# Performance work log

Hardware: AMD Instinct MI355X
Metric: run time of the kernel (lower is better)

## Reference

```python
import jax, jax.numpy as jnp
import numpy as np

B, T, S, K, H, V = 8, 100, 400, 8, 512, 32000

def setup_inputs() -> dict:
    key = jax.random.key(0)
    ks = jax.random.split(key, 8)
    return {
        "dec_out": jax.random.normal(ks[0], (B, T, H), jnp.float32),
        "W": jax.random.normal(ks[1], (H, V), jnp.float32) * (1.0 / np.sqrt(H)),
        "b": jnp.zeros((V,), jnp.float32),
        "weights": jax.random.uniform(ks[2], (B, T, S), jnp.float32),
        "p_trans": jax.random.uniform(ks[3], (B, T, 1), jnp.float32),
        "trans_probs": jax.random.uniform(ks[4], (B, S, K), jnp.float32),
        "probs": jax.random.uniform(ks[5], (B, S, K), jnp.float32),
        "idxes": jax.random.randint(ks[6], (B, S, K), 0, V, jnp.int64),
    }

def reference(dec_out, W, b, weights, p_trans, trans_probs, probs, idxes):
    # Generator: linear + softmax over vocab -> (B, T, V)
    scores = jax.nn.softmax(jnp.einsum('bth,hv->btv', dec_out, W) + b, axis=-1)
    # Mask translation probs where source prob <= 0.05
    tp = trans_probs * (probs > 0.05).astype(trans_probs.dtype)  # (B, S, K)
    # scatter_add along vocab dim: tmp[b, s, idxes[b, s, k]] += tp[b, s, k]
    bi = jnp.arange(B)[:, None, None]
    si = jnp.arange(S)[None, :, None]
    tmp = jnp.zeros((B, S, V), dec_out.dtype).at[bi, si, idxes].add(tp)
    # blend copy distribution through attention weights
    trans_scores = jnp.einsum('bts,bsv->btv', weights, tmp)
    return jnp.log(p_trans * trans_scores + (1.0 - p_trans) * scores)
```

## Files before the change

kernel.cpp:

```cpp
#include <hip/hip_runtime.h>

#define Bdim 8
#define Tdim 100
#define Sdim 400
#define Kk   8
#define Hdim 512
#define Vdim 32000
#define Mdim 800
#define VHALF 16000

typedef __attribute__((ext_vector_type(8))) short short8;
typedef __attribute__((ext_vector_type(4))) short short4v;
typedef __attribute__((ext_vector_type(4))) float float4_t;

static __device__ __forceinline__ unsigned short f2bf(float f) {
    unsigned int x = __float_as_uint(f);
    return (unsigned short)((x + 0x7fffu + ((x >> 16) & 1u)) >> 16);
}
static __device__ __forceinline__ float bf2f(unsigned short h) {
    return __uint_as_float(((unsigned int)h) << 16);
}

static __device__ __forceinline__ void gload_lds16(const void* g, void* s) {
    __builtin_amdgcn_global_load_lds((const __attribute__((address_space(1))) void*)g,
                                     (__attribute__((address_space(3))) void*)s, 16, 0, 0);
}

__global__ void zero_kernel(float* __restrict__ p, int n) {
    int i = blockIdx.x * blockDim.x + threadIdx.x;
    if (i < n) p[i] = 0.f;
}

__global__ void convert_a_kernel(const float* __restrict__ A, unsigned short* __restrict__ Abf, int n4) {
    int i = blockIdx.x * blockDim.x + threadIdx.x;
    if (i < n4) {
        float4 f = ((const float4*)A)[i];
        short4v s;
        s[0] = (short)f2bf(f.x); s[1] = (short)f2bf(f.y);
        s[2] = (short)f2bf(f.z); s[3] = (short)f2bf(f.w);
        *(short4v*)(Abf + i * 4) = s;
    }
}

__global__ __launch_bounds__(256) void transpose_kernel(const float* __restrict__ W,
                                                        unsigned short* __restrict__ WT) {
    __shared__ float tile[64][65];
    const int k0 = blockIdx.y * 64;
    const int v0 = blockIdx.x * 64;
    const int t  = threadIdx.x;
    const int tx = t & 15;
    const int ty = t >> 4;
#pragma unroll
    for (int i = 0; i < 64; i += 16) {
        float4 f = *(const float4*)&W[(size_t)(k0 + ty + i) * Vdim + v0 + tx * 4];
        tile[ty + i][tx * 4 + 0] = f.x;
        tile[ty + i][tx * 4 + 1] = f.y;
        tile[ty + i][tx * 4 + 2] = f.z;
        tile[ty + i][tx * 4 + 3] = f.w;
    }
    __syncthreads();
    const int c = t & 7;
    const int v = t >> 3;
#pragma unroll
    for (int i = 0; i < 64; i += 32) {
        short8 s;
#pragma unroll
        for (int j = 0; j < 8; ++j) s[j] = (short)f2bf(tile[c * 8 + j][v + i]);
        *(short8*)&WT[(size_t)(v0 + v + i) * Hdim + k0 + c * 8] = s;
    }
}

__global__ __launch_bounds__(256) void gemm_kernel(const unsigned short* __restrict__ Abf,
                                                   const unsigned short* __restrict__ WT,
                                                   const float* __restrict__ bias,
                                                   unsigned short* __restrict__ logitsbf,
                                                   float* __restrict__ rowsum) {
    __shared__ __align__(16) unsigned short As[2 * 128 * 64];
    __shared__ __align__(16) unsigned short Bs[2 * 128 * 64];

    const int tid  = threadIdx.x;
    const int lane = tid & 63;
    const int wave = tid >> 6;
    const int l15  = lane & 15;
    const int kq   = lane >> 4;

    const int NWG = 7 * 250;
    const int orig = blockIdx.x;
    const int xcd = orig & 7;
    const int q8  = NWG >> 3;
    const int r8  = NWG & 7;
    const int wg  = (xcd < r8 ? xcd * (q8 + 1) : r8 * (q8 + 1) + (xcd - r8) * q8) + (orig >> 3);
    const int m_blk = (wg % 7) * 128;
    const int n_blk = (wg / 7) * 128;

    const int wm = wave & 1, wn = wave >> 1;
    const int m0 = wm * 64, n0 = wn * 64;

    const unsigned short* agp[4];
    const unsigned short* bgp[4];
    int lslot[4];
#pragma unroll
    for (int q = 0; q < 4; ++q) {
        int chunk = (q * 4 + wave) * 64 + lane;
        int row = chunk >> 3, c = chunk & 7;
        int gc  = c ^ (row & 7);
        int arow = m_blk + row;
        if (arow >= Mdim) arow = Mdim - 1;
        agp[q] = Abf + (size_t)arow * Hdim + gc * 8;
        bgp[q] = WT + (size_t)(n_blk + row) * Hdim + gc * 8;
        lslot[q] = (q * 4 + wave) * 512;
    }

    int a_off[2][4], b_off[2][4];
#pragma unroll
    for (int ks = 0; ks < 2; ++ks)
#pragma unroll
        for (int i = 0; i < 4; ++i) {
            int ra = m0 + i * 16 + l15;
            a_off[ks][i] = ra * 64 + (((ks * 4 + kq) ^ (ra & 7)) * 8);
            int rb = n0 + i * 16 + l15;
            b_off[ks][i] = rb * 64 + (((ks * 4 + kq) ^ (rb & 7)) * 8);
        }

    float4_t acc[4][4] = {};

#pragma unroll
    for (int q = 0; q < 4; ++q) {
        gload_lds16(agp[q], As + lslot[q]);
        gload_lds16(bgp[q], Bs + lslot[q]);
    }
    __syncthreads();

    int cur = 0;
#pragma unroll
    for (int kt = 0; kt < 8; ++kt) {
        if (kt < 7) {
            const int ko = (kt + 1) * 64;
            const int nb = (cur ^ 1) * 8192;
#pragma unroll
            for (int q = 0; q < 4; ++q) {
                gload_lds16(agp[q] + ko, As + nb + lslot[q]);
                gload_lds16(bgp[q] + ko, Bs + nb + lslot[q]);
            }
        }
        const unsigned short* Ab = As + cur * 8192;
        const unsigned short* Bb = Bs + cur * 8192;
#pragma unroll
        for (int ks = 0; ks < 2; ++ks) {
            short8 af[4], bfr[4];
#pragma unroll
            for (int i = 0; i < 4; ++i) af[i]  = *(const short8*)(Ab + a_off[ks][i]);
#pragma unroll
            for (int j = 0; j < 4; ++j) bfr[j] = *(const short8*)(Bb + b_off[ks][j]);
#pragma unroll
            for (int i = 0; i < 4; ++i)
#pragma unroll
                for (int j = 0; j < 4; ++j)
                    acc[i][j] = __builtin_amdgcn_mfma_f32_16x16x32_bf16(af[i], bfr[j], acc[i][j], 0, 0, 0);
        }
        if (kt < 7) {
            __syncthreads();
            cur ^= 1;
        }
    }

    float bj[4];
#pragma unroll
    for (int j = 0; j < 4; ++j) bj[j] = bias[n_blk + n0 + j * 16 + l15];

#pragma unroll
    for (int i = 0; i < 4; ++i) {
        float se[4] = {0.f, 0.f, 0.f, 0.f};
        int grow0 = m_blk + m0 + i * 16 + kq * 4;
#pragma unroll
        for (int j = 0; j < 4; ++j) {
            int col = n_blk + n0 + j * 16 + l15;
#pragma unroll
            for (int r = 0; r < 4; ++r) {
                float v = acc[i][j][r] + bj[j];
                se[r] += __expf(v);
                if (grow0 + r < Mdim)
                    logitsbf[(size_t)(grow0 + r) * Vdim + col] = f2bf(v);
            }
        }
#pragma unroll
        for (int r = 0; r < 4; ++r) {
#pragma unroll
            for (int off = 8; off; off >>= 1)
                se[r] += __shfl_xor(se[r], off, 64);
        }
        if (l15 == 0) {
#pragma unroll
            for (int r = 0; r < 4; ++r)
                if (grow0 + r < Mdim) atomicAdd(&rowsum[grow0 + r], se[r]);
        }
    }
}

__global__ __launch_bounds__(512) void combine_kernel(const unsigned short* __restrict__ logitsbf,
                                                      const float* __restrict__ weights,
                                                      const float* __restrict__ p_trans,
                                                      const float* __restrict__ trans_probs,
                                                      const float* __restrict__ probs,
                                                      const int* __restrict__ idxes,
                                                      const float* __restrict__ rowsum,
                                                      float* __restrict__ out) {
    __shared__ __align__(16) float ts[VHALF];

    int bt = blockIdx.x;
    int b  = bt / Tdim;
    int tid = threadIdx.x;

    float pt = p_trans[bt];
    float c1 = (1.f - pt) / rowsum[bt];

    const short8* lrow8 = (const short8*)(logitsbf + (size_t)bt * Vdim);
    float4* out4 = (float4*)(out + (size_t)bt * Vdim);
    float4* ts4  = (float4*)ts;

    for (int h = 0; h < 2; ++h) {
        float4 z = make_float4(0.f, 0.f, 0.f, 0.f);
        for (int i = tid; i < VHALF / 4; i += 512) ts4[i] = z;
        __syncthreads();

        for (int i = tid; i < Sdim * Kk; i += 512) {
            float pv  = probs[b * (Sdim * Kk) + i];
            float tpv = trans_probs[b * (Sdim * Kk) + i];
            int   idx = idxes[b * (Sdim * Kk) + i];
            int   rel = idx - h * VHALF;
            if (pv > 0.05f && (unsigned)rel < (unsigned)VHALF) {
                float w = weights[bt * Sdim + (i >> 3)];
                atomicAdd(&ts[rel], w * tpv);
            }
        }
        __syncthreads();

        for (int i = tid; i < VHALF / 8; i += 512) {
            short8 x8 = lrow8[h * (VHALF / 8) + i];
            float4 t0 = ts4[i * 2];
            float4 t1 = ts4[i * 2 + 1];
            float4 o0, o1;
            o0.x = __logf(pt * t0.x + c1 * __expf(bf2f((unsigned short)x8[0])));
            o0.y = __logf(pt * t0.y + c1 * __expf(bf2f((unsigned short)x8[1])));
            o0.z = __logf(pt * t0.z + c1 * __expf(bf2f((unsigned short)x8[2])));
            o0.w = __logf(pt * t0.w + c1 * __expf(bf2f((unsigned short)x8[3])));
            o1.x = __logf(pt * t1.x + c1 * __expf(bf2f((unsigned short)x8[4])));
            o1.y = __logf(pt * t1.y + c1 * __expf(bf2f((unsigned short)x8[5])));
            o1.z = __logf(pt * t1.z + c1 * __expf(bf2f((unsigned short)x8[6])));
            o1.w = __logf(pt * t1.w + c1 * __expf(bf2f((unsigned short)x8[7])));
            out4[(h * (VHALF / 8) + i) * 2]     = o0;
            out4[(h * (VHALF / 8) + i) * 2 + 1] = o1;
        }
        __syncthreads();
    }
}

extern "C" void kernel_launch(void* const* d_in, const int* in_sizes, int n_in,
                              void* d_out, int out_size, void* d_ws, size_t ws_size,
                              hipStream_t stream) {
    const float* dec_out     = (const float*)d_in[0];
    const float* W           = (const float*)d_in[1];
    const float* bias        = (const float*)d_in[2];
    const float* weights     = (const float*)d_in[3];
    const float* p_trans     = (const float*)d_in[4];
    const float* trans_probs = (const float*)d_in[5];
    const float* probs       = (const float*)d_in[6];
    const int*   idxes       = (const int*)d_in[7];
    float* out = (float*)d_out;

    char* wsb = (char*)d_ws;
    unsigned short* Abf      = (unsigned short*)wsb;
    unsigned short* WT       = (unsigned short*)(wsb + (1ull << 20));
    unsigned short* logitsbf = (unsigned short*)(wsb + (35ull << 20));
    float*          rowsum   = (float*)(wsb + (90ull << 20));

    zero_kernel<<<dim3(4), dim3(256), 0, stream>>>(rowsum, Mdim);
    convert_a_kernel<<<dim3((Mdim * Hdim / 4 + 255) / 256), dim3(256), 0, stream>>>(dec_out, Abf, Mdim * Hdim / 4);
    transpose_kernel<<<dim3(Vdim / 64, Hdim / 64), dim3(256), 0, stream>>>(W, WT);
    gemm_kernel<<<dim3(7 * (Vdim / 128)), dim3(256), 0, stream>>>(Abf, WT, bias, logitsbf, rowsum);
    combine_kernel<<<dim3(Mdim), dim3(512), 0, stream>>>(logitsbf, weights, p_trans, trans_probs,
                                                         probs, idxes, rowsum, out);
}
```

Measured before the change: 284.7 us.

## Enlarge GEMM tiles to 256x256 with 512 threads and fold rowsum zeroing

The GEMM tile grows from 128x128 to 256x256, launched as 500 workgroups of 512 threads, with each wave computing a 128x64 sub-tile. The aim is to raise arithmetic intensity and cut redundant B/W reads. The per-iteration sync is rebuilt as an explicit vmcnt wait plus a barrier at the top of each k step, and A fragments are loaded one at a time to limit register pressure. The zero kernel is folded into convert_a to save a launch. The cost is more padded M rows (1024 versus 800), higher register and LDS use, and fewer workgroups to spread across CUs.

```diff
diff --git a/kernel.cpp b/kernel.cpp
--- a/kernel.cpp
+++ b/kernel.cpp
@@ -26,13 +26,10 @@
                                      (__attribute__((address_space(3))) void*)s, 16, 0, 0);
 }
 
-__global__ void zero_kernel(float* __restrict__ p, int n) {
+__global__ void convert_a_kernel(const float* __restrict__ A, unsigned short* __restrict__ Abf,
+                                 float* __restrict__ rowsum, int n4) {
     int i = blockIdx.x * blockDim.x + threadIdx.x;
-    if (i < n) p[i] = 0.f;
-}
-
-__global__ void convert_a_kernel(const float* __restrict__ A, unsigned short* __restrict__ Abf, int n4) {
-    int i = blockIdx.x * blockDim.x + threadIdx.x;
+    if (i < Mdim) rowsum[i] = 0.f;
     if (i < n4) {
         float4 f = ((const float4*)A)[i];
         short4v s;
@@ -70,13 +67,13 @@
     }
 }
 
-__global__ __launch_bounds__(256) void gemm_kernel(const unsigned short* __restrict__ Abf,
-                                                   const unsigned short* __restrict__ WT,
-                                                   const float* __restrict__ bias,
-                                                   unsigned short* __restrict__ logitsbf,
-                                                   float* __restrict__ rowsum) {
-    __shared__ __align__(16) unsigned short As[2 * 128 * 64];
-    __shared__ __align__(16) unsigned short Bs[2 * 128 * 64];
+__global__ __launch_bounds__(512, 2) void gemm_kernel(const unsigned short* __restrict__ Abf,
+                                                      const unsigned short* __restrict__ WT,
+                                                      const float* __restrict__ bias,
+                                                      unsigned short* __restrict__ logitsbf,
+                                                      float* __restrict__ rowsum) {
+    __shared__ __align__(16) unsigned short As[2 * 256 * 64];
+    __shared__ __align__(16) unsigned short Bs[2 * 256 * 64];
 
     const int tid  = threadIdx.x;
     const int lane = tid & 63;
@@ -84,84 +81,87 @@
     const int l15  = lane & 15;
     const int kq   = lane >> 4;
 
-    const int NWG = 7 * 250;
+    const int NWG = 500;
     const int orig = blockIdx.x;
     const int xcd = orig & 7;
     const int q8  = NWG >> 3;
     const int r8  = NWG & 7;
     const int wg  = (xcd < r8 ? xcd * (q8 + 1) : r8 * (q8 + 1) + (xcd - r8) * q8) + (orig >> 3);
-    const int m_blk = (wg % 7) * 128;
-    const int n_blk = (wg / 7) * 128;
+    const int m_blk = (wg & 3) * 256;
+    const int n_blk = (wg >> 2) * 256;
 
     const int wm = wave & 1, wn = wave >> 1;
-    const int m0 = wm * 64, n0 = wn * 64;
+    const int m0 = wm * 128, n0 = wn * 64;
 
     const unsigned short* agp[4];
     const unsigned short* bgp[4];
     int lslot[4];
 #pragma unroll
     for (int q = 0; q < 4; ++q) {
-        int chunk = (q * 4 + wave) * 64 + lane;
+        int chunk = (q * 8 + wave) * 64 + lane;
         int row = chunk >> 3, c = chunk & 7;
         int gc  = c ^ (row & 7);
         int arow = m_blk + row;
         if (arow >= Mdim) arow = Mdim - 1;
         agp[q] = Abf + (size_t)arow * Hdim + gc * 8;
         bgp[q] = WT + (size_t)(n_blk + row) * Hdim + gc * 8;
-        lslot[q] = (q * 4 + wave) * 512;
-    }
-
-    int a_off[2][4], b_off[2][4];
-#pragma unroll
-    for (int ks = 0; ks < 2; ++ks)
-#pragma unroll
-        for (int i = 0; i < 4; ++i) {
+        lslot[q] = (q * 8 + wave) * 512;
+    }
+
+    int a_off[2][8], b_off[2][4];
+#pragma unroll
+    for (int ks = 0; ks < 2; ++ks) {
+#pragma unroll
+        for (int i = 0; i < 8; ++i) {
             int ra = m0 + i * 16 + l15;
             a_off[ks][i] = ra * 64 + (((ks * 4 + kq) ^ (ra & 7)) * 8);
-            int rb = n0 + i * 16 + l15;
-            b_off[ks][i] = rb * 64 + (((ks * 4 + kq) ^ (rb & 7)) * 8);
-        }
-
-    float4_t acc[4][4] = {};
+        }
+#pragma unroll
+        for (int j = 0; j < 4; ++j) {
+            int rb = n0 + j * 16 + l15;
+            b_off[ks][j] = rb * 64 + (((ks * 4 + kq) ^ (rb & 7)) * 8);
+        }
+    }
+
+    float4_t acc[8][4] = {};
 
 #pragma unroll
     for (int q = 0; q < 4; ++q) {
         gload_lds16(agp[q], As + lslot[q]);
         gload_lds16(bgp[q], Bs + lslot[q]);
     }
-    __syncthreads();
 
     int cur = 0;
 #pragma unroll
     for (int kt = 0; kt < 8; ++kt) {
+        asm volatile("s_waitcnt vmcnt(0)" ::: "memory");
+        __builtin_amdgcn_s_barrier();
+        __builtin_amdgcn_sched_barrier(0);
         if (kt < 7) {
             const int ko = (kt + 1) * 64;
-            const int nb = (cur ^ 1) * 8192;
+            const int nb = (cur ^ 1) * 16384;
 #pragma unroll
             for (int q = 0; q < 4; ++q) {
                 gload_lds16(agp[q] + ko, As + nb + lslot[q]);
                 gload_lds16(bgp[q] + ko, Bs + nb + lslot[q]);
             }
         }
-        const unsigned short* Ab = As + cur * 8192;
-        const unsigned short* Bb = Bs + cur * 8192;
+        const unsigned short* Ab = As + cur * 16384;
+        const unsigned short* Bb = Bs + cur * 16384;
 #pragma unroll
         for (int ks = 0; ks < 2; ++ks) {
-            short8 af[4], bfr[4];
-#pragma unroll
-            for (int i = 0; i < 4; ++i) af[i]  = *(const short8*)(Ab + a_off[ks][i]);
+            short8 bfr[4];
 #pragma unroll
             for (int j = 0; j < 4; ++j) bfr[j] = *(const short8*)(Bb + b_off[ks][j]);
 #pragma unroll
-            for (int i = 0; i < 4; ++i)
+            for (int i = 0; i < 8; ++i) {
+                short8 af = *(const short8*)(Ab + a_off[ks][i]);
 #pragma unroll
                 for (int j = 0; j < 4; ++j)
-                    acc[i][j] = __builtin_amdgcn_mfma_f32_16x16x32_bf16(af[i], bfr[j], acc[i][j], 0, 0, 0);
-        }
-        if (kt < 7) {
-            __syncthreads();
-            cur ^= 1;
-        }
+                    acc[i][j] = __builtin_amdgcn_mfma_f32_16x16x32_bf16(af, bfr[j], acc[i][j], 0, 0, 0);
+            }
+        }
+        cur ^= 1;
     }
 
     float bj[4];
@@ -169,7 +169,7 @@
     for (int j = 0; j < 4; ++j) bj[j] = bias[n_blk + n0 + j * 16 + l15];
 
 #pragma unroll
-    for (int i = 0; i < 4; ++i) {
+    for (int i = 0; i < 8; ++i) {
         float se[4] = {0.f, 0.f, 0.f, 0.f};
         int grow0 = m_blk + m0 + i * 16 + kq * 4;
 #pragma unroll
@@ -274,10 +274,9 @@
     unsigned short* logitsbf = (unsigned short*)(wsb + (35ull << 20));
     float*          rowsum   = (float*)(wsb + (90ull << 20));
 
-    zero_kernel<<<dim3(4), dim3(256), 0, stream>>>(rowsum, Mdim);
-    convert_a_kernel<<<dim3((Mdim * Hdim / 4 + 255) / 256), dim3(256), 0, stream>>>(dec_out, Abf, Mdim * Hdim / 4);
+    convert_a_kernel<<<dim3((Mdim * Hdim / 4 + 255) / 256), dim3(256), 0, stream>>>(dec_out, Abf, rowsum, Mdim * Hdim / 4);
     transpose_kernel<<<dim3(Vdim / 64, Hdim / 64), dim3(256), 0, stream>>>(W, WT);
-    gemm_kernel<<<dim3(7 * (Vdim / 128)), dim3(256), 0, stream>>>(Abf, WT, bias, logitsbf, rowsum);
+    gemm_kernel<<<dim3(500), dim3(512), 0, stream>>>(Abf, WT, bias, logitsbf, rowsum);
     combine_kernel<<<dim3(Mdim), dim3(512), 0, stream>>>(logitsbf, weights, p_trans, trans_probs,
                                                          probs, idxes, rowsum, out);
 }
```

Result: slower. 302.4 us (+6.2%).

## Split combine over vocab chunks, fold rowsum zeroing, restructure GEMM barriers

Applied to the files above, without the earlier changes.

The combine kernel now runs on a 2D grid of rows by 4000-wide vocab chunks with 256 threads, so each block has a small LDS scatter buffer instead of looping over two 16000-wide halves. This raises parallelism and occupancy. In exchange, every chunk block rescans all 3200 (s,k) index entries for its batch, which adds redundant global reads and filtering. The rowsum zeroing moves into the convert kernel, removing one launch. The GEMM loop replaces __syncthreads with an explicit vmcnt wait plus barrier at the top of each iteration.

```diff
diff --git a/kernel.cpp b/kernel.cpp
--- a/kernel.cpp
+++ b/kernel.cpp
@@ -7,7 +7,7 @@
 #define Hdim 512
 #define Vdim 32000
 #define Mdim 800
-#define VHALF 16000
+#define VCHUNK 4000
 
 typedef __attribute__((ext_vector_type(8))) short short8;
 typedef __attribute__((ext_vector_type(4))) short short4v;
@@ -26,13 +26,10 @@
                                      (__attribute__((address_space(3))) void*)s, 16, 0, 0);
 }
 
-__global__ void zero_kernel(float* __restrict__ p, int n) {
+__global__ void convert_a_kernel(const float* __restrict__ A, unsigned short* __restrict__ Abf,
+                                 float* __restrict__ rowsum, int n4) {
     int i = blockIdx.x * blockDim.x + threadIdx.x;
-    if (i < n) p[i] = 0.f;
-}
-
-__global__ void convert_a_kernel(const float* __restrict__ A, unsigned short* __restrict__ Abf, int n4) {
-    int i = blockIdx.x * blockDim.x + threadIdx.x;
+    if (i < Mdim) rowsum[i] = 0.f;
     if (i < n4) {
         float4 f = ((const float4*)A)[i];
         short4v s;
@@ -129,11 +126,13 @@
         gload_lds16(agp[q], As + lslot[q]);
         gload_lds16(bgp[q], Bs + lslot[q]);
     }
-    __syncthreads();
 
     int cur = 0;
 #pragma unroll
     for (int kt = 0; kt < 8; ++kt) {
+        asm volatile("s_waitcnt vmcnt(0)" ::: "memory");
+        __builtin_amdgcn_s_barrier();
+        __builtin_amdgcn_sched_barrier(0);
         if (kt < 7) {
             const int ko = (kt + 1) * 64;
             const int nb = (cur ^ 1) * 8192;
@@ -158,10 +157,7 @@
                 for (int j = 0; j < 4; ++j)
                     acc[i][j] = __builtin_amdgcn_mfma_f32_16x16x32_bf16(af[i], bfr[j], acc[i][j], 0, 0, 0);
         }
-        if (kt < 7) {
-            __syncthreads();
-            cur ^= 1;
-        }
+        cur ^= 1;
     }
 
     float bj[4];
@@ -197,7 +193,7 @@
     }
 }
 
-__global__ __launch_bounds__(512) void combine_kernel(const unsigned short* __restrict__ logitsbf,
+__global__ __launch_bounds__(256) void combine_kernel(const unsigned short* __restrict__ logitsbf,
                                                       const float* __restrict__ weights,
                                                       const float* __restrict__ p_trans,
                                                       const float* __restrict__ trans_probs,
@@ -205,53 +201,53 @@
                                                       const int* __restrict__ idxes,
                                                       const float* __restrict__ rowsum,
                                                       float* __restrict__ out) {
-    __shared__ __align__(16) float ts[VHALF];
-
-    int bt = blockIdx.x;
-    int b  = bt / Tdim;
-    int tid = threadIdx.x;
-
-    float pt = p_trans[bt];
-    float c1 = (1.f - pt) / rowsum[bt];
-
-    const short8* lrow8 = (const short8*)(logitsbf + (size_t)bt * Vdim);
-    float4* out4 = (float4*)(out + (size_t)bt * Vdim);
-    float4* ts4  = (float4*)ts;
-
-    for (int h = 0; h < 2; ++h) {
-        float4 z = make_float4(0.f, 0.f, 0.f, 0.f);
-        for (int i = tid; i < VHALF / 4; i += 512) ts4[i] = z;
-        __syncthreads();
-
-        for (int i = tid; i < Sdim * Kk; i += 512) {
-            float pv  = probs[b * (Sdim * Kk) + i];
-            float tpv = trans_probs[b * (Sdim * Kk) + i];
-            int   idx = idxes[b * (Sdim * Kk) + i];
-            int   rel = idx - h * VHALF;
-            if (pv > 0.05f && (unsigned)rel < (unsigned)VHALF) {
-                float w = weights[bt * Sdim + (i >> 3)];
-                atomicAdd(&ts[rel], w * tpv);
-            }
-        }
-        __syncthreads();
-
-        for (int i = tid; i < VHALF / 8; i += 512) {
-            short8 x8 = lrow8[h * (VHALF / 8) + i];
-            float4 t0 = ts4[i * 2];
-            float4 t1 = ts4[i * 2 + 1];
-            float4 o0, o1;
-            o0.x = __logf(pt * t0.x + c1 * __expf(bf2f((unsigned short)x8[0])));
-            o0.y = __logf(pt * t0.y + c1 * __expf(bf2f((unsigned short)x8[1])));
-            o0.z = __logf(pt * t0.z + c1 * __expf(bf2f((unsigned short)x8[2])));
-            o0.w = __logf(pt * t0.w + c1 * __expf(bf2f((unsigned short)x8[3])));
-            o1.x = __logf(pt * t1.x + c1 * __expf(bf2f((unsigned short)x8[4])));
-            o1.y = __logf(pt * t1.y + c1 * __expf(bf2f((unsigned short)x8[5])));
-            o1.z = __logf(pt * t1.z + c1 * __expf(bf2f((unsigned short)x8[6])));
-            o1.w = __logf(pt * t1.w + c1 * __expf(bf2f((unsigned short)x8[7])));
-            out4[(h * (VHALF / 8) + i) * 2]     = o0;
-            out4[(h * (VHALF / 8) + i) * 2 + 1] = o1;
-        }
-        __syncthreads();
+    __shared__ __align__(16) float ts[VCHUNK];
+
+    const int bt  = blockIdx.x;
+    const int c   = blockIdx.y;
+    const int b   = bt / Tdim;
+    const int tid = threadIdx.x;
+    const int v0  = c * VCHUNK;
+
+    const float pt = p_trans[bt];
+    const float c1 = (1.f - pt) / rowsum[bt];
+
+    float4* ts4 = (float4*)ts;
+    const float4 z = make_float4(0.f, 0.f, 0.f, 0.f);
+#pragma unroll
+    for (int i = tid; i < VCHUNK / 4; i += 256) ts4[i] = z;
+    __syncthreads();
+
+    for (int i = tid; i < Sdim * Kk; i += 256) {
+        float pv  = probs[b * (Sdim * Kk) + i];
+        float tpv = trans_probs[b * (Sdim * Kk) + i];
+        int   idx = idxes[b * (Sdim * Kk) + i];
+        int   rel = idx - v0;
+        if (pv > 0.05f && (unsigned)rel < (unsigned)VCHUNK) {
+            float w = weights[bt * Sdim + (i >> 3)];
+            atomicAdd(&ts[rel], w * tpv);
+        }
+    }
+    __syncthreads();
+
+    const short8* lrow8 = (const short8*)(logitsbf + (size_t)bt * Vdim + v0);
+    float4* out4 = (float4*)(out + (size_t)bt * Vdim + v0);
+#pragma unroll
+    for (int i = tid; i < VCHUNK / 8; i += 256) {
+        short8 x8 = lrow8[i];
+        float4 t0 = ts4[i * 2];
+        float4 t1 = ts4[i * 2 + 1];
+        float4 o0, o1;
+        o0.x = __logf(pt * t0.x + c1 * __expf(bf2f((unsigned short)x8[0])));
+        o0.y = __logf(pt * t0.y + c1 * __expf(bf2f((unsigned short)x8[1])));
+        o0.z = __logf(pt * t0.z + c1 * __expf(bf2f((unsigned short)x8[2])));
+        o0.w = __logf(pt * t0.w + c1 * __expf(bf2f((unsigned short)x8[3])));
+        o1.x = __logf(pt * t1.x + c1 * __expf(bf2f((unsigned short)x8[4])));
+        o1.y = __logf(pt * t1.y + c1 * __expf(bf2f((unsigned short)x8[5])));
+        o1.z = __logf(pt * t1.z + c1 * __expf(bf2f((unsigned short)x8[6])));
+        o1.w = __logf(pt * t1.w + c1 * __expf(bf2f((unsigned short)x8[7])));
+        out4[i * 2]     = o0;
+        out4[i * 2 + 1] = o1;
     }
 }
 
@@ -274,10 +270,9 @@
     unsigned short* logitsbf = (unsigned short*)(wsb + (35ull << 20));
     float*          rowsum   = (float*)(wsb + (90ull << 20));
 
-    zero_kernel<<<dim3(4), dim3(256), 0, stream>>>(rowsum, Mdim);
-    convert_a_kernel<<<dim3((Mdim * Hdim / 4 + 255) / 256), dim3(256), 0, stream>>>(dec_out, Abf, Mdim * Hdim / 4);
+    convert_a_kernel<<<dim3((Mdim * Hdim / 4 + 255) / 256), dim3(256), 0, stream>>>(dec_out, Abf, rowsum, Mdim * Hdim / 4);
     transpose_kernel<<<dim3(Vdim / 64, Hdim / 64), dim3(256), 0, stream>>>(W, WT);
-    gemm_kernel<<<dim3(7 * (Vdim / 128)), dim3(256), 0, stream>>>(Abf, WT, bias, logitsbf, rowsum);
-    combine_kernel<<<dim3(Mdim), dim3(512), 0, stream>>>(logitsbf, weights, p_trans, trans_probs,
-                                                         probs, idxes, rowsum, out);
-}
+    gemm_kernel<<<dim3(7 * 250), dim3(256), 0, stream>>>(Abf, WT, bias, logitsbf, rowsum);
+    combine_kernel<<<dim3(Mdim, Vdim / VCHUNK), dim3(256), 0, stream>>>(logitsbf, weights, p_trans, trans_probs,
+                                                                        probs, idxes, rowsum, out);
+}
```

Measured after the change: 286.8 us. No clear change (+0.7%).
